# Kernel optimization log

Hardware: AMD Instinct MI355X
Metric: run time of the kernel (lower is better)

Reference implementation:

```python
import jax, jax.numpy as jnp
import numpy as np

N_NODES = 10000
N_EDGES = 160000
N_GRAPHS = 64
F = 80        # hidden dim
T = 5         # towers
F_OUT = 16    # per-tower post output (80/5)
N_LAYERS = 4
EPS = 1e-6
BN_EPS = 1e-5
STD_EPS = 1e-5


def setup_inputs() -> dict:
    key = jax.random.key(0)
    ks = jax.random.split(key, 12)
    x = jax.random.uniform(ks[0], (N_NODES, 2), dtype=jnp.float32)
    edge_index = jax.random.randint(ks[1], (2, N_EDGES), 0, N_NODES, dtype=jnp.int64)
    batch = jnp.sort(jax.random.randint(ks[2], (N_NODES,), 0, N_GRAPHS, dtype=jnp.int64))

    def w(k, shape, fan_in):
        return (jax.random.normal(k, shape, jnp.float32) / np.float32(np.sqrt(fan_in)))

    return {
        "x": x, "edge_index": edge_index, "batch": batch,
        "pre_lin_W": w(ks[3], (1, F), 1), "pre_lin_b": jnp.zeros((F,), jnp.float32),
        "pre_W": w(ks[4], (N_LAYERS, T, 2 * F, F), 2 * F), "pre_b": jnp.zeros((N_LAYERS, T, F), jnp.float32),
        "post_W": w(ks[5], (N_LAYERS, T, 13 * F, F_OUT), 13 * F), "post_b": jnp.zeros((N_LAYERS, T, F_OUT), jnp.float32),
        "lin_W": w(ks[6], (N_LAYERS, F, F), F), "lin_b": jnp.zeros((N_LAYERS, F), jnp.float32),
        "bn_gamma": jnp.ones((N_LAYERS, F), jnp.float32), "bn_beta": jnp.zeros((N_LAYERS, F), jnp.float32),
        "mlp_lin_W": w(ks[7], (40, 1), 40), "mlp_lin_b": jnp.zeros((1,), jnp.float32),
        "mlp1_W": w(ks[8], (40, 20), 40), "mlp1_b": jnp.zeros((20,), jnp.float32),
        "mlp2_W": w(ks[9], (20, 1), 20), "mlp2_b": jnp.zeros((1,), jnp.float32),
    }


def _pna_conv(h, src, dst, deg, avg_log_deg, preW, preb, postW, postb, linW, linb):
    # h: [N, F]; messages per tower: pre MLP over cat(x_i, x_j)  (divide_input=False)
    N = h.shape[0]
    hm = jnp.concatenate([h[dst], h[src]], axis=-1)            # [E, 2F]
    m = jnp.einsum('ef,tfo->eto', hm, preW) + preb             # [E, T, F]

    cnt = jnp.maximum(deg, 1.0)[:, None, None]                 # [N,1,1]
    has = (deg > 0)[:, None, None]
    s = jax.ops.segment_sum(m, dst, num_segments=N)
    mean = s / cnt
    mean_sq = jax.ops.segment_sum(m * m, dst, num_segments=N) / cnt
    mn = jax.ops.segment_min(m, dst, num_segments=N)
    mx = jax.ops.segment_max(m, dst, num_segments=N)
    mn = jnp.where(has, mn, 0.0)
    mx = jnp.where(has, mx, 0.0)
    std = jnp.sqrt(jax.nn.relu(mean_sq - mean * mean) + STD_EPS)
    agg = jnp.concatenate([mean, mn, mx, std], axis=-1)        # [N, T, 4F]

    logd = jnp.log(jnp.maximum(deg, 1.0) + 1.0)[:, None, None]
    amp = agg * (logd / avg_log_deg)
    att = agg * (avg_log_deg / logd)
    out = jnp.concatenate([agg, amp, att], axis=-1)            # [N, T, 12F]

    xt = jnp.broadcast_to(h[:, None, :], (N, T, F))
    out = jnp.concatenate([xt, out], axis=-1)                  # [N, T, 13F]
    out = jnp.einsum('ntf,tfo->nto', out, postW) + postb       # [N, T, F_OUT]
    out = out.reshape(N, T * F_OUT)                            # [N, 80]
    return out @ linW + linb


def _forward(x, edge_index, batch, pre_lin_W, pre_lin_b, pre_W, pre_b,
             post_W, post_b, lin_W, lin_b, bn_gamma, bn_beta,
             mlp_lin_W, mlp_lin_b, mlp1_W, mlp1_b, mlp2_W, mlp2_b):
    N = x.shape[0]
    src, dst = edge_index[0], edge_index[1]
    deg = jax.ops.segment_sum(jnp.ones_like(dst, jnp.float32), dst, num_segments=N)
    avg_log_deg = jnp.mean(jnp.log(deg + 1.0))                 # PNA avg log-degree from deg histogram

    operation = x[:, 0:1]
    assignment = x[:, 1:2]
    op = operation @ pre_lin_W + pre_lin_b                     # [N, 80]

    for l in range(N_LAYERS):
        y = _pna_conv(op, src, dst, deg, avg_log_deg,
                      pre_W[l], pre_b[l], post_W[l], post_b[l], lin_W[l], lin_b[l])
        mu = jnp.mean(y, axis=0)
        var = jnp.mean((y - mu) ** 2, axis=0)                  # biased, training-mode BN
        y = (y - mu) / jnp.sqrt(var + BN_EPS) * bn_gamma[l] + bn_beta[l]
        op = jax.nn.relu(y)

    front, behind = op[:, :40], op[:, 40:]
    xc = front * assignment + behind                           # [N, 40], non-negative

    # LastLayer: log-space scatter-add message passing
    log_score = jax.ops.segment_sum(jnp.log(xc[src] + EPS), dst, num_segments=N)
    xc = jnp.exp(log_score + jnp.log(xc + EPS))

    # global mean pool over graphs
    gcnt = jnp.maximum(jax.ops.segment_sum(jnp.ones_like(batch, jnp.float32), batch, num_segments=N_GRAPHS), 1.0)
    pooled = jax.ops.segment_sum(xc, batch, num_segments=N_GRAPHS) / gcnt[:, None]  # [B, 40]

    x_lin = pooled @ mlp_lin_W + mlp_lin_b
    x_cv = pooled @ mlp1_W + mlp1_b
    x_cv = 20.0 - jax.nn.relu(x_cv)
    x_cv = x_cv @ mlp2_W + mlp2_b
    return x_cv + x_lin                                        # [B, 1]


def reference(x, edge_index, batch, pre_lin_W, pre_lin_b, pre_W, pre_b,
              post_W, post_b, lin_W, lin_b, bn_gamma, bn_beta,
              mlp_lin_W, mlp_lin_b, mlp1_W, mlp1_b, mlp2_W, mlp2_b):
    return _forward(x, edge_index, batch, pre_lin_W, pre_lin_b, pre_W, pre_b,
                    post_W, post_b, lin_W, lin_b, bn_gamma, bn_beta,
                    mlp_lin_W, mlp_lin_b, mlp1_W, mlp1_b, mlp2_W, mlp2_b)
```

## Files before the change

kernel.cpp:

```cpp
#include <hip/hip_runtime.h>
#include <math.h>

#define NN 10000
#define NE 160000
#define NG 64
#define FEAT 80
#define NT 5
#define NL 4

__global__ void k_count(const int* __restrict__ dst, int* __restrict__ deg) {
    int e = blockIdx.x * 256 + threadIdx.x;
    if (e < NE) atomicAdd(&deg[dst[e]], 1);
}

__global__ void k_gcnt(const int* __restrict__ batch, int* __restrict__ gcnt) {
    int n = blockIdx.x * 256 + threadIdx.x;
    if (n < NN) atomicAdd(&gcnt[batch[n]], 1);
}

__global__ void k_scan(const int* __restrict__ deg, int* __restrict__ offs) {
    __shared__ int sums[256];
    int tid = threadIdx.x;
    int start = tid * 40, stop = min(start + 40, NN);
    int s = 0;
    for (int i = start; i < stop; ++i) s += deg[i];
    sums[tid] = s;
    __syncthreads();
    for (int off = 1; off < 256; off <<= 1) {
        int v = (tid >= off) ? sums[tid - off] : 0;
        __syncthreads();
        sums[tid] += v;
        __syncthreads();
    }
    int base = (tid == 0) ? 0 : sums[tid - 1];
    for (int i = start; i < stop; ++i) { offs[i] = base; base += deg[i]; }
    if (tid == 255) offs[NN] = sums[255];
}

__global__ void k_ald(const int* __restrict__ deg, float* __restrict__ ald) {
    __shared__ float red[256];
    int i = blockIdx.x * 256 + threadIdx.x;
    red[threadIdx.x] = (i < NN) ? logf((float)deg[i] + 1.0f) : 0.0f;
    __syncthreads();
    for (int s = 128; s > 0; s >>= 1) {
        if (threadIdx.x < s) red[threadIdx.x] += red[threadIdx.x + s];
        __syncthreads();
    }
    if (threadIdx.x == 0) atomicAdd(ald, red[0]);
}

__global__ void k_fill(const int* __restrict__ src, const int* __restrict__ dst,
                       const int* __restrict__ offs, int* __restrict__ cursor,
                       int* __restrict__ csr) {
    int e = blockIdx.x * 256 + threadIdx.x;
    if (e < NE) {
        int d = dst[e];
        int p = atomicAdd(&cursor[d], 1);
        csr[offs[d] + p] = src[e];
    }
}

__global__ void k_op0(const float* __restrict__ x, const float* __restrict__ plW,
                      const float* __restrict__ plb, float* __restrict__ hT) {
    int i = blockIdx.x * 256 + threadIdx.x;
    if (i < FEAT * NN) {
        int f = i / NN, n = i - f * NN;
        hT[i] = x[2 * n] * plW[f] + plb[f];
    }
}

__global__ __launch_bounds__(256) void k_mm_ab(
        const float* __restrict__ hT, const float* __restrict__ preW_l,
        float* __restrict__ A, float* __restrict__ Bt) {
    __shared__ float hs[16][80];
    int n0 = blockIdx.x * 16;
    int tid = threadIdx.x;
    for (int i = tid; i < 16 * 80; i += 256) {
        int nl = i & 15, f = i >> 4;
        hs[nl][f] = hT[(size_t)f * NN + n0 + nl];
    }
    __syncthreads();
    int c0 = blockIdx.y * 512 + tid;
    float acc[2][16];
#pragma unroll
    for (int s = 0; s < 2; s++)
#pragma unroll
        for (int i = 0; i < 16; i++) acc[s][i] = 0.f;
    const float* wp[2];
#pragma unroll
    for (int s = 0; s < 2; s++) {
        int c = c0 + s * 256;
        int part = (c >= 400) ? 1 : 0;
        int cc = c - part * 400;
        int t = cc / 80, o = cc - t * 80;
        wp[s] = preW_l + (size_t)(t * 160 + part * 80) * 80 + o;
    }
    bool act1 = (c0 + 256) < 800;
    for (int fq = 0; fq < 80; fq += 4) {
        float w0a = wp[0][(fq + 0) * 80], w0b = wp[0][(fq + 1) * 80];
        float w0c = wp[0][(fq + 2) * 80], w0d = wp[0][(fq + 3) * 80];
        float w1a = 0.f, w1b = 0.f, w1c = 0.f, w1d = 0.f;
        if (act1) {
            w1a = wp[1][(fq + 0) * 80]; w1b = wp[1][(fq + 1) * 80];
            w1c = wp[1][(fq + 2) * 80]; w1d = wp[1][(fq + 3) * 80];
        }
#pragma unroll
        for (int i = 0; i < 16; i++) {
            float4 hv = *(const float4*)&hs[i][fq];
            acc[0][i] += hv.x * w0a + hv.y * w0b + hv.z * w0c + hv.w * w0d;
            acc[1][i] += hv.x * w1a + hv.y * w1b + hv.z * w1c + hv.w * w1d;
        }
    }
#pragma unroll
    for (int s = 0; s < 2; s++) {
        int c = c0 + s * 256;
        if (c < 800) {
            int part = (c >= 400) ? 1 : 0;
            int cc = c - part * 400;
            int t = cc / 80, o = cc - t * 80;
            if (part == 0) {
#pragma unroll
                for (int i = 0; i < 16; i++) A[(size_t)(n0 + i) * 400 + cc] = acc[s][i];
            } else {
#pragma unroll
                for (int i = 0; i < 16; i++)
                    Bt[((size_t)t * NN + n0 + i) * 80 + o] = acc[s][i];
            }
        }
    }
}

__global__ __launch_bounds__(256) void k_agg_t(
        const float* __restrict__ A, const float* __restrict__ Bt,
        const int* __restrict__ offs, const int* __restrict__ csr,
        const float* __restrict__ preb_l, float* __restrict__ aggT) {
    __shared__ float st[320 * 17];
    int tid = threadIdx.x;
    int t = blockIdx.y;
    int n0 = blockIdx.x * 16;
    int ni = tid >> 4;
    int cl = tid & 15;
    int n = n0 + ni;
    int e0 = offs[n], e1 = offs[n + 1];
    const float* Bts = Bt + (size_t)t * NN * 80;
    float s[5], q[5], mn[5], mx[5];
#pragma unroll
    for (int k = 0; k < 5; k++) { s[k] = 0.f; q[k] = 0.f; mn[k] = 3.4e38f; mx[k] = -3.4e38f; }
    int e = e0;
    for (; e + 3 < e1; e += 4) {
        const float* br0 = Bts + (size_t)csr[e] * 80 + cl;
        const float* br1 = Bts + (size_t)csr[e + 1] * 80 + cl;
        const float* br2 = Bts + (size_t)csr[e + 2] * 80 + cl;
        const float* br3 = Bts + (size_t)csr[e + 3] * 80 + cl;
#pragma unroll
        for (int k = 0; k < 5; k++) {
            float b0 = br0[k * 16];
            float b1 = br1[k * 16];
            float b2 = br2[k * 16];
            float b3 = br3[k * 16];
            s[k] += (b0 + b1) + (b2 + b3);
            q[k] += (b0 * b0 + b1 * b1) + (b2 * b2 + b3 * b3);
            mn[k] = fminf(mn[k], fminf(fminf(b0, b1), fminf(b2, b3)));
            mx[k] = fmaxf(mx[k], fmaxf(fmaxf(b0, b1), fmaxf(b2, b3)));
        }
    }
    for (; e < e1; ++e) {
        const float* br = Bts + (size_t)csr[e] * 80 + cl;
#pragma unroll
        for (int k = 0; k < 5; k++) {
            float b = br[k * 16];
            s[k] += b; q[k] += b * b;
            mn[k] = fminf(mn[k], b); mx[k] = fmaxf(mx[k], b);
        }
    }
    int d = e1 - e0;
    float degf = (float)d;
    float cnt = fmaxf(degf, 1.f);
#pragma unroll
    for (int k = 0; k < 5; k++) {
        int c = cl + k * 16;
        float a = A[(size_t)n * 400 + t * 80 + c] + preb_l[t * 80 + c];
        float mean = (degf * a + s[k]) / cnt;
        float msq  = (degf * a * a + 2.f * a * s[k] + q[k]) / cnt;
        float sd = sqrtf(fmaxf(msq - mean * mean, 0.f) + 1e-5f);
        float mnr = (d > 0) ? a + mn[k] : 0.f;
        float mxr = (d > 0) ? a + mx[k] : 0.f;
        st[(0 * 80 + c) * 17 + ni] = mean;
        st[(1 * 80 + c) * 17 + ni] = mnr;
        st[(2 * 80 + c) * 17 + ni] = mxr;
        st[(3 * 80 + c) * 17 + ni] = sd;
    }
    __syncthreads();
    int jj = tid >> 4;
    int nl = tid & 15;
#pragma unroll
    for (int pass = 0; pass < 20; ++pass) {
        int j = pass * 16 + jj;
        aggT[((size_t)t * 320 + j) * NN + n0 + nl] = st[j * 17 + nl];
    }
}

__global__ __launch_bounds__(256) void k_post(
        const float* __restrict__ hT, const float* __restrict__ aggT,
        const float* __restrict__ postW_l, const float* __restrict__ postb_l,
        const int* __restrict__ offs, const float* __restrict__ ald_sum,
        float* __restrict__ y0T) {
    __shared__ float wj[40 * 48];
    __shared__ float wh[80 * 16];
    int tid = threadIdx.x;
    int t = blockIdx.y;
    int jq = blockIdx.z;
    int j0 = jq * 40;
    const float* W0 = postW_l + (size_t)t * 1040 * 16;
    const float* W1 = W0 + 80 * 16;
    const float* W2 = W0 + 400 * 16;
    const float* W3 = W0 + 720 * 16;
    for (int idx = tid; idx < 40 * 48; idx += 256) {
        int j = idx / 48;
        int rem = idx - j * 48;
        int p = rem >> 4, o = rem & 15;
        const float* Wp = (p == 0) ? W1 : (p == 1) ? W2 : W3;
        wj[idx] = Wp[(j0 + j) * 16 + o];
    }
    if (jq == 0) {
        for (int idx = tid; idx < 80 * 16; idx += 256)
            wh[idx] = W0[idx];
    }
    __syncthreads();
    int n = blockIdx.x * 256 + tid;
    bool alive = (n < NN);
    int nc = alive ? n : 0;
    float acc1[16], acc2[16], acc3[16];
#pragma unroll
    for (int i = 0; i < 16; i++) { acc1[i] = 0.f; acc2[i] = 0.f; acc3[i] = 0.f; }
    const float* ap = aggT + ((size_t)t * 320 + j0) * NN + nc;
#pragma unroll 8
    for (int j = 0; j < 40; ++j) {
        float a = ap[(size_t)j * NN];
        const float* w = wj + j * 48;
#pragma unroll
        for (int i = 0; i < 16; i++) {
            acc1[i] += a * w[i];
            acc2[i] += a * w[16 + i];
            acc3[i] += a * w[32 + i];
        }
    }
    if (jq == 0) {
#pragma unroll 4
        for (int f = 0; f < 80; ++f) {
            float hv = hT[(size_t)f * NN + nc];
            const float* w = wh + f * 16;
#pragma unroll
            for (int i = 0; i < 16; i++) acc1[i] += hv * w[i];
        }
    }
    if (alive) {
        float degf = (float)(offs[n + 1] - offs[n]);
        float ald = ald_sum[0] * (1.f / NN);
        float logd = logf(fmaxf(degf, 1.f) + 1.f);
        float c1 = logd / ald;
        float c2 = ald / logd;
#pragma unroll
        for (int i = 0; i < 16; i++) {
            float v = acc1[i] + c1 * acc2[i] + c2 * acc3[i];
            if (jq == 0) v += postb_l[t * 16 + i];
            unsafeAtomicAdd(&y0T[(size_t)(t * 16 + i) * NN + n], v);
        }
    }
}

__global__ __launch_bounds__(256) void k_lin(
        const float* __restrict__ y0T, const float* __restrict__ linW_l,
        const float* __restrict__ linb_l, float* __restrict__ yT) {
    __shared__ float ws[80 * 8];
    int tid = threadIdx.x;
    int f0 = blockIdx.y * 8;
    for (int idx = tid; idx < 80 * 8; idx += 256)
        ws[idx] = linW_l[(idx >> 3) * 80 + f0 + (idx & 7)];
    __syncthreads();
    int n = blockIdx.x * 256 + tid;
    bool alive = (n < NN);
    int nc = alive ? n : 0;
    float acc[8];
#pragma unroll
    for (int i = 0; i < 8; i++) acc[i] = 0.f;
#pragma unroll 8
    for (int k = 0; k < 80; ++k) {
        float v = y0T[(size_t)k * NN + nc];
        const float4 wa = *(const float4*)(ws + k * 8);
        const float4 wb = *(const float4*)(ws + k * 8 + 4);
        acc[0] += v * wa.x; acc[1] += v * wa.y; acc[2] += v * wa.z; acc[3] += v * wa.w;
        acc[4] += v * wb.x; acc[5] += v * wb.y; acc[6] += v * wb.z; acc[7] += v * wb.w;
    }
    if (alive) {
#pragma unroll
        for (int i = 0; i < 8; i++)
            yT[(size_t)(f0 + i) * NN + n] = acc[i] + linb_l[f0 + i];
    }
}

__global__ void k_bnstats(const float* __restrict__ yT, float* __restrict__ bnst) {
    __shared__ float r1[256], r2[256];
    int f = blockIdx.x;
    int tid = threadIdx.x;
    float s = 0.f, q = 0.f;
    for (int i = tid; i < NN; i += 256) {
        float v = yT[(size_t)f * NN + i];
        s += v; q += v * v;
    }
    r1[tid] = s; r2[tid] = q;
    __syncthreads();
    for (int st = 128; st > 0; st >>= 1) {
        if (tid < st) { r1[tid] += r1[tid + st]; r2[tid] += r2[tid + st]; }
        __syncthreads();
    }
    if (tid == 0) { bnst[f] = r1[0]; bnst[80 + f] = r2[0]; }
}

__global__ void k_bn(const float* __restrict__ yT, const float* __restrict__ bnst,
                     const float* __restrict__ gamma_l, const float* __restrict__ beta_l,
                     float* __restrict__ hT) {
    int i = blockIdx.x * 256 + threadIdx.x;
    if (i >= FEAT * NN) return;
    int f = i / NN;
    float mu = bnst[f] * (1.f / NN);
    float msq = bnst[80 + f] * (1.f / NN);
    float var = fmaxf(msq - mu * mu, 0.f);
    float v = (yT[i] - mu) * (1.f / sqrtf(var + 1e-5f)) * gamma_l[f] + beta_l[f];
    hT[i] = fmaxf(v, 0.f);
}

__global__ void k_xc(const float* __restrict__ hT, const float* __restrict__ x,
                     float* __restrict__ lxc) {
    int i = blockIdx.x * 256 + threadIdx.x;
    if (i >= 40 * NN) return;
    int j = i / NN, n = i - j * NN;
    float v = hT[(size_t)j * NN + n] * x[2 * n + 1] + hT[(size_t)(40 + j) * NN + n];
    lxc[(size_t)n * 40 + j] = logf(v + 1e-6f);
}

__global__ void k_logagg(const float* __restrict__ lxc, const int* __restrict__ offs,
                         const int* __restrict__ csr, const int* __restrict__ batch,
                         float* __restrict__ pooled) {
    int n = blockIdx.x;
    int tid = threadIdx.x;
    if (tid >= 40) return;
    int e0 = offs[n], e1 = offs[n + 1];
    float s = 0.f;
    for (int k = e0; k < e1; ++k) s += lxc[(size_t)csr[k] * 40 + tid];
    float v = expf(s + lxc[(size_t)n * 40 + tid]);
    atomicAdd(&pooled[batch[n] * 40 + tid], v);
}

__global__ void k_final(const float* __restrict__ pooled, const int* __restrict__ gcnt,
                        const float* __restrict__ mlW, const float* __restrict__ mlb,
                        const float* __restrict__ m1W, const float* __restrict__ m1b,
                        const float* __restrict__ m2W, const float* __restrict__ m2b,
                        float* __restrict__ out) {
    int g = threadIdx.x;
    if (g >= NG) return;
    float inv = 1.f / fmaxf((float)gcnt[g], 1.f);
    float pl[40];
#pragma unroll
    for (int j = 0; j < 40; j++) pl[j] = pooled[g * 40 + j] * inv;
    float xl = mlb[0];
#pragma unroll
    for (int j = 0; j < 40; j++) xl += pl[j] * mlW[j];
    float acc = m2b[0];
    for (int k = 0; k < 20; k++) {
        float v = m1b[k];
#pragma unroll
        for (int j = 0; j < 40; j++) v += pl[j] * m1W[j * 20 + k];
        v = 20.f - fmaxf(v, 0.f);
        acc += v * m2W[k];
    }
    out[g] = acc + xl;
}

extern "C" void kernel_launch(void* const* d_in, const int* in_sizes, int n_in,
                              void* d_out, int out_size, void* d_ws, size_t ws_size,
                              hipStream_t stream) {
    const float* x     = (const float*)d_in[0];
    const int*   ei    = (const int*)d_in[1];
    const int*   batch = (const int*)d_in[2];
    const float* plW   = (const float*)d_in[3];
    const float* plb   = (const float*)d_in[4];
    const float* preW  = (const float*)d_in[5];
    const float* preb  = (const float*)d_in[6];
    const float* postW = (const float*)d_in[7];
    const float* postb = (const float*)d_in[8];
    const float* linW  = (const float*)d_in[9];
    const float* linb  = (const float*)d_in[10];
    const float* bnG   = (const float*)d_in[11];
    const float* bnB   = (const float*)d_in[12];
    const float* mlW   = (const float*)d_in[13];
    const float* mlb   = (const float*)d_in[14];
    const float* m1W   = (const float*)d_in[15];
    const float* m1b   = (const float*)d_in[16];
    const float* m2W   = (const float*)d_in[17];
    const float* m2b   = (const float*)d_in[18];
    float* out = (float*)d_out;
    const int* srcp = ei;
    const int* dstp = ei + NE;

    char* p = (char*)d_ws;
    int*   deg    = (int*)(p + 0);
    int*   cursor = (int*)(p + 40000);
    int*   gcnt   = (int*)(p + 80000);
    float* ald    = (float*)(p + 80256);
    float* pooled = (float*)(p + 80272);
    float* bnst   = (float*)(p + 90512);
    int*   offs   = (int*)(p + 93072);
    int*   csr    = (int*)(p + 133088);
    float* hT     = (float*)(p + 773088);
    float* A      = (float*)(p + 3973088);
    float* Bt     = (float*)(p + 19973088);
    float* aggT   = (float*)(p + 35973088);
    float* y0T = (float*)(p + 23173088);
    float* yT  = (float*)(p + 26373088);
    float* lxc = (float*)(p + 35973088);

    hipMemsetAsync(d_ws, 0, 90512, stream);
    k_count<<<dim3((NE + 255) / 256), 256, 0, stream>>>(dstp, deg);
    k_gcnt<<<dim3((NN + 255) / 256), 256, 0, stream>>>(batch, gcnt);
    k_scan<<<1, 256, 0, stream>>>(deg, offs);
    k_ald<<<dim3((NN + 255) / 256), 256, 0, stream>>>(deg, ald);
    k_fill<<<dim3((NE + 255) / 256), 256, 0, stream>>>(srcp, dstp, offs, cursor, csr);
    k_op0<<<dim3((FEAT * NN + 255) / 256), 256, 0, stream>>>(x, plW, plb, hT);

    for (int l = 0; l < NL; ++l) {
        const float* preW_l  = preW  + (size_t)l * NT * 160 * 80;
        const float* preb_l  = preb  + l * NT * 80;
        const float* postW_l = postW + (size_t)l * NT * 1040 * 16;
        const float* postb_l = postb + l * NT * 16;
        const float* linW_l  = linW  + l * 80 * 80;
        const float* linb_l  = linb  + l * 80;
        float* bnst_l = bnst + l * 160;
        k_mm_ab<<<dim3(625, 2), 256, 0, stream>>>(hT, preW_l, A, Bt);
        k_agg_t<<<dim3(625, 5), 256, 0, stream>>>(A, Bt, offs, csr, preb_l, aggT);
        hipMemsetAsync(y0T, 0, (size_t)80 * NN * 4, stream);
        k_post<<<dim3(40, 5, 8), 256, 0, stream>>>(hT, aggT, postW_l, postb_l, offs, ald, y0T);
        k_lin<<<dim3(40, 10), 256, 0, stream>>>(y0T, linW_l, linb_l, yT);
        k_bnstats<<<dim3(80), 256, 0, stream>>>(yT, bnst_l);
        k_bn<<<dim3((FEAT * NN + 255) / 256), 256, 0, stream>>>(yT, bnst_l, bnG + l * 80, bnB + l * 80, hT);
    }

    k_xc<<<dim3((40 * NN + 255) / 256), 256, 0, stream>>>(hT, x, lxc);
    k_logagg<<<dim3(NN), 64, 0, stream>>>(lxc, offs, csr, batch, pooled);
    k_final<<<1, 64, 0, stream>>>(pooled, gcnt, mlW, mlb, m1W, m1b, m2W, m2b, out);
}
```

Baseline: 873.5 us.

## Fold post-MLP h-term and bias into lin layer; process two nodes per thread in k_post

Precomputes per layer a combined 80x80 weight (post_W h-slice times lin_W) and a combined bias in a new small kernel. k_lin then applies it directly to hT, so the jq==0 blocks of k_post no longer do an extra 80-feature pass and those blocks stop being imbalanced. k_post also now handles two nodes per thread with 48 accumulators each and hoists the degree scalers into shared memory, reusing shared weights across more nodes. The cost is an extra tiny launch per layer, an extra 80-term loop in k_lin, and higher register pressure in k_post.

```diff
diff --git a/kernel.cpp b/kernel.cpp
--- a/kernel.cpp
+++ b/kernel.cpp
@@ -201,20 +201,18 @@
 }
 
 __global__ __launch_bounds__(256) void k_post(
-        const float* __restrict__ hT, const float* __restrict__ aggT,
-        const float* __restrict__ postW_l, const float* __restrict__ postb_l,
+        const float* __restrict__ aggT, const float* __restrict__ postW_l,
         const int* __restrict__ offs, const float* __restrict__ ald_sum,
         float* __restrict__ y0T) {
     __shared__ float wj[40 * 48];
-    __shared__ float wh[80 * 16];
+    __shared__ float c1s[512], c2s[512];
     int tid = threadIdx.x;
     int t = blockIdx.y;
     int jq = blockIdx.z;
     int j0 = jq * 40;
-    const float* W0 = postW_l + (size_t)t * 1040 * 16;
-    const float* W1 = W0 + 80 * 16;
-    const float* W2 = W0 + 400 * 16;
-    const float* W3 = W0 + 720 * 16;
+    const float* W1 = postW_l + (size_t)t * 1040 * 16 + 80 * 16;
+    const float* W2 = W1 + 320 * 16;
+    const float* W3 = W2 + 320 * 16;
     for (int idx = tid; idx < 40 * 48; idx += 256) {
         int j = idx / 48;
         int rem = idx - j * 48;
@@ -222,61 +220,91 @@
         const float* Wp = (p == 0) ? W1 : (p == 1) ? W2 : W3;
         wj[idx] = Wp[(j0 + j) * 16 + o];
     }
-    if (jq == 0) {
-        for (int idx = tid; idx < 80 * 16; idx += 256)
-            wh[idx] = W0[idx];
-    }
-    __syncthreads();
-    int n = blockIdx.x * 256 + tid;
-    bool alive = (n < NN);
-    int nc = alive ? n : 0;
-    float acc1[16], acc2[16], acc3[16];
-#pragma unroll
-    for (int i = 0; i < 16; i++) { acc1[i] = 0.f; acc2[i] = 0.f; acc3[i] = 0.f; }
-    const float* ap = aggT + ((size_t)t * 320 + j0) * NN + nc;
-#pragma unroll 8
+    int n0 = blockIdx.x * 512;
+    float ald = ald_sum[0] * (1.f / NN);
+    for (int i = tid; i < 512; i += 256) {
+        int n = n0 + i;
+        if (n < NN) {
+            float degf = (float)(offs[n + 1] - offs[n]);
+            float logd = logf(fmaxf(degf, 1.f) + 1.f);
+            c1s[i] = logd / ald;
+            c2s[i] = ald / logd;
+        }
+    }
+    __syncthreads();
+    int na = n0 + tid;
+    int nb = n0 + 256 + tid;
+    bool ala = (na < NN), alb = (nb < NN);
+    int nca = ala ? na : 0;
+    int ncb = alb ? nb : 0;
+    float acca[48], accb[48];
+#pragma unroll
+    for (int i = 0; i < 48; i++) { acca[i] = 0.f; accb[i] = 0.f; }
+    const float* ap = aggT + ((size_t)t * 320 + j0) * NN;
+#pragma unroll 2
     for (int j = 0; j < 40; ++j) {
-        float a = ap[(size_t)j * NN];
+        float a0 = ap[(size_t)j * NN + nca];
+        float a1 = ap[(size_t)j * NN + ncb];
         const float* w = wj + j * 48;
 #pragma unroll
-        for (int i = 0; i < 16; i++) {
-            acc1[i] += a * w[i];
-            acc2[i] += a * w[16 + i];
-            acc3[i] += a * w[32 + i];
-        }
-    }
-    if (jq == 0) {
-#pragma unroll 4
-        for (int f = 0; f < 80; ++f) {
-            float hv = hT[(size_t)f * NN + nc];
-            const float* w = wh + f * 16;
-#pragma unroll
-            for (int i = 0; i < 16; i++) acc1[i] += hv * w[i];
-        }
-    }
-    if (alive) {
-        float degf = (float)(offs[n + 1] - offs[n]);
-        float ald = ald_sum[0] * (1.f / NN);
-        float logd = logf(fmaxf(degf, 1.f) + 1.f);
-        float c1 = logd / ald;
-        float c2 = ald / logd;
-#pragma unroll
-        for (int i = 0; i < 16; i++) {
-            float v = acc1[i] + c1 * acc2[i] + c2 * acc3[i];
-            if (jq == 0) v += postb_l[t * 16 + i];
-            unsafeAtomicAdd(&y0T[(size_t)(t * 16 + i) * NN + n], v);
-        }
+        for (int i = 0; i < 48; i++) {
+            acca[i] += a0 * w[i];
+            accb[i] += a1 * w[i];
+        }
+    }
+    if (ala) {
+        float c1 = c1s[tid], c2 = c2s[tid];
+#pragma unroll
+        for (int o = 0; o < 16; o++) {
+            float v = acca[o] + c1 * acca[16 + o] + c2 * acca[32 + o];
+            unsafeAtomicAdd(&y0T[(size_t)(t * 16 + o) * NN + na], v);
+        }
+    }
+    if (alb) {
+        float c1 = c1s[256 + tid], c2 = c2s[256 + tid];
+#pragma unroll
+        for (int o = 0; o < 16; o++) {
+            float v = accb[o] + c1 * accb[16 + o] + c2 * accb[32 + o];
+            unsafeAtomicAdd(&y0T[(size_t)(t * 16 + o) * NN + nb], v);
+        }
+    }
+}
+
+__global__ void k_wh(const float* __restrict__ postW_l, const float* __restrict__ linW_l,
+                     const float* __restrict__ postb_l, const float* __restrict__ linb_l,
+                     float* __restrict__ Wh, float* __restrict__ linb2) {
+    int f = blockIdx.x;
+    int fo = threadIdx.x;
+    if (fo >= 80) return;
+    if (f < 80) {
+        float s = 0.f;
+        for (int t = 0; t < NT; ++t) {
+            const float* w0 = postW_l + ((size_t)t * 1040 + f) * 16;
+#pragma unroll
+            for (int o2 = 0; o2 < 16; ++o2)
+                s += w0[o2] * linW_l[(t * 16 + o2) * 80 + fo];
+        }
+        Wh[f * 80 + fo] = s;
+    } else {
+        float s = linb_l[fo];
+        for (int k = 0; k < 80; ++k)
+            s += postb_l[k] * linW_l[k * 80 + fo];
+        linb2[fo] = s;
     }
 }
 
 __global__ __launch_bounds__(256) void k_lin(
-        const float* __restrict__ y0T, const float* __restrict__ linW_l,
-        const float* __restrict__ linb_l, float* __restrict__ yT) {
+        const float* __restrict__ y0T, const float* __restrict__ hT,
+        const float* __restrict__ linW_l, const float* __restrict__ Wh,
+        const float* __restrict__ linb2, float* __restrict__ yT) {
     __shared__ float ws[80 * 8];
+    __shared__ float whs[80 * 8];
     int tid = threadIdx.x;
     int f0 = blockIdx.y * 8;
-    for (int idx = tid; idx < 80 * 8; idx += 256)
-        ws[idx] = linW_l[(idx >> 3) * 80 + f0 + (idx & 7)];
+    for (int idx = tid; idx < 80 * 8; idx += 256) {
+        ws[idx]  = linW_l[(idx >> 3) * 80 + f0 + (idx & 7)];
+        whs[idx] = Wh[(idx >> 3) * 80 + f0 + (idx & 7)];
+    }
     __syncthreads();
     int n = blockIdx.x * 256 + tid;
     bool alive = (n < NN);
@@ -292,10 +320,18 @@
         acc[0] += v * wa.x; acc[1] += v * wa.y; acc[2] += v * wa.z; acc[3] += v * wa.w;
         acc[4] += v * wb.x; acc[5] += v * wb.y; acc[6] += v * wb.z; acc[7] += v * wb.w;
     }
+#pragma unroll 8
+    for (int k = 0; k < 80; ++k) {
+        float v = hT[(size_t)k * NN + nc];
+        const float4 wa = *(const float4*)(whs + k * 8);
+        const float4 wb = *(const float4*)(whs + k * 8 + 4);
+        acc[0] += v * wa.x; acc[1] += v * wa.y; acc[2] += v * wa.z; acc[3] += v * wa.w;
+        acc[4] += v * wb.x; acc[5] += v * wb.y; acc[6] += v * wb.z; acc[7] += v * wb.w;
+    }
     if (alive) {
 #pragma unroll
         for (int i = 0; i < 8; i++)
-            yT[(size_t)(f0 + i) * NN + n] = acc[i] + linb_l[f0 + i];
+            yT[(size_t)(f0 + i) * NN + n] = acc[i] + linb2[f0 + i];
     }
 }
 
@@ -416,9 +452,11 @@
     float* A      = (float*)(p + 3973088);
     float* Bt     = (float*)(p + 19973088);
     float* aggT   = (float*)(p + 35973088);
-    float* y0T = (float*)(p + 23173088);
-    float* yT  = (float*)(p + 26373088);
-    float* lxc = (float*)(p + 35973088);
+    float* y0T   = (float*)(p + 23173088);
+    float* yT    = (float*)(p + 26373088);
+    float* Wh    = (float*)(p + 29573088);
+    float* linb2 = (float*)(p + 29598688);
+    float* lxc   = (float*)(p + 35973088);
 
     hipMemsetAsync(d_ws, 0, 90512, stream);
     k_count<<<dim3((NE + 255) / 256), 256, 0, stream>>>(dstp, deg);
@@ -437,10 +475,11 @@
         const float* linb_l  = linb  + l * 80;
         float* bnst_l = bnst + l * 160;
         k_mm_ab<<<dim3(625, 2), 256, 0, stream>>>(hT, preW_l, A, Bt);
+        k_wh<<<dim3(81), 128, 0, stream>>>(postW_l, linW_l, postb_l, linb_l, Wh, linb2);
         k_agg_t<<<dim3(625, 5), 256, 0, stream>>>(A, Bt, offs, csr, preb_l, aggT);
         hipMemsetAsync(y0T, 0, (size_t)80 * NN * 4, stream);
-        k_post<<<dim3(40, 5, 8), 256, 0, stream>>>(hT, aggT, postW_l, postb_l, offs, ald, y0T);
-        k_lin<<<dim3(40, 10), 256, 0, stream>>>(y0T, linW_l, linb_l, yT);
+        k_post<<<dim3(20, 5, 8), 256, 0, stream>>>(aggT, postW_l, offs, ald, y0T);
+        k_lin<<<dim3(40, 10), 256, 0, stream>>>(y0T, hT, linW_l, Wh, linb2, yT);
         k_bnstats<<<dim3(80), 256, 0, stream>>>(yT, bnst_l);
         k_bn<<<dim3((FEAT * NN + 255) / 256), 256, 0, stream>>>(yT, bnst_l, bnG + l * 80, bnB + l * 80, hT);
     }
```

Result: slower. 948.1 us (+8.5%).
